# Kernel tuning notes

Hardware: AMD Instinct MI355X
Metric: run time of the kernel (lower is better)

The kernel has to match this reference:

```python
import jax, jax.numpy as jnp
import numpy as np

NH, NKV, HD = 32, 8, 64      # query heads, kv heads, head dim
H, INTER = 2048, 8192        # hidden, mlp intermediate
B, NBLK, BS = 32, 256, 16    # batch, blocks per seq, block size
NUM_BLOCKS = B * NBLK
EPS = 1e-5
THETA = 10000.0


def rms_norm(x, w):
    var = jnp.mean(x * x, axis=-1, keepdims=True)
    return x * jax.lax.rsqrt(var + EPS) * w


def rotate_half(x):
    x1, x2 = jnp.split(x, 2, axis=-1)
    return jnp.concatenate([-x2, x1], axis=-1)


def setup_inputs() -> dict:
    key = jax.random.key(0)
    ks = jax.random.split(key, 12)
    s = 0.02
    x = jax.random.normal(ks[0], (B, 1, H), jnp.float32)
    k_cache = jax.random.normal(ks[1], (NUM_BLOCKS, BS, NKV, HD), jnp.float32)
    v_cache = jax.random.normal(ks[2], (NUM_BLOCKS, BS, NKV, HD), jnp.float32)
    block_table = jnp.arange(B * NBLK, dtype=jnp.int32).reshape(B, NBLK)
    cache_seqlens = jax.random.randint(ks[3], (B,), 0, NBLK * BS - 1, jnp.int32)
    return {
        'x': x, 'k_cache': k_cache, 'v_cache': v_cache,
        'ln1_w': jnp.ones((H,), jnp.float32),
        'q_w': jax.random.normal(ks[4], (H, NH * HD), jnp.float32) * s,
        'k_w': jax.random.normal(ks[5], (H, NKV * HD), jnp.float32) * s,
        'v_w': jax.random.normal(ks[6], (H, NKV * HD), jnp.float32) * s,
        'o_w': jax.random.normal(ks[7], (NH * HD, H), jnp.float32) * s,
        'ln2_w': jnp.ones((H,), jnp.float32),
        'gate_w': jax.random.normal(ks[8], (H, INTER), jnp.float32) * s,
        'up_w': jax.random.normal(ks[9], (H, INTER), jnp.float32) * s,
        'down_w': jax.random.normal(ks[10], (INTER, H), jnp.float32) * s,
        'block_table': block_table,
        'cache_seqlens': cache_seqlens,
        'block_size': BS,
    }


def reference(x, k_cache, v_cache, ln1_w, q_w, k_w, v_w, o_w, ln2_w,
              gate_w, up_w, down_w, block_table, cache_seqlens, block_size):
    b = x.shape[0]
    normed = rms_norm(x, ln1_w)[:, 0, :]                     # [B,H]
    q = (normed @ q_w).reshape(b, NH, HD)                    # [B,NH,HD]
    k = (normed @ k_w).reshape(b, NKV, HD)                   # [B,NKV,HD]
    v = (normed @ v_w).reshape(b, NKV, HD)

    # RoPE at current position (HF rotate_half convention)
    pos = cache_seqlens.astype(jnp.float32)                  # [B]
    inv_freq = 1.0 / (THETA ** (jnp.arange(0, HD, 2, dtype=jnp.float32) / HD))
    ang = pos[:, None] * inv_freq[None, :]                   # [B,HD/2]
    cos = jnp.concatenate([jnp.cos(ang), jnp.cos(ang)], -1)[:, None, :]  # [B,1,HD]
    sin = jnp.concatenate([jnp.sin(ang), jnp.sin(ang)], -1)[:, None, :]
    q = q * cos + rotate_half(q) * sin
    k = k * cos + rotate_half(k) * sin

    # paged cache update: write new k/v at block_table[b, pos//bs], offset pos%bs
    blk = block_table[jnp.arange(b), cache_seqlens // block_size]
    flat_idx = blk.astype(jnp.int32) * block_size + cache_seqlens % block_size  # [B]
    kc = k_cache.reshape(-1, NKV, HD).at[flat_idx].set(k).reshape(k_cache.shape)
    vc = v_cache.reshape(-1, NKV, HD).at[flat_idx].set(v).reshape(v_cache.shape)

    # gather paged KV via block table -> [B, S, NKV, HD]
    K = kc[block_table].reshape(b, -1, NKV, HD)
    V = vc[block_table].reshape(b, -1, NKV, HD)
    S = K.shape[1]

    # decode attention with GQA: head h uses kv head h // (NH//NKV)
    G = NH // NKV
    qh = q.reshape(b, NKV, G, HD)
    scores = jnp.einsum('bkgd,bskd->bkgs', qh, K) / jnp.sqrt(jnp.float32(HD))
    valid = (jnp.arange(S)[None, :] <= cache_seqlens[:, None])  # seqlen+1 tokens
    scores = jnp.where(valid[:, None, None, :], scores, -jnp.inf)
    probs = jax.nn.softmax(scores, axis=-1)
    attn = jnp.einsum('bkgs,bskd->bkgd', probs, V).reshape(b, NH * HD)

    x = x + (attn @ o_w)[:, None, :]

    h = rms_norm(x, ln2_w)
    mlp = (jax.nn.silu(h @ gate_w) * (h @ up_w)) @ down_w
    return x + mlp
```

## Files before the change

kernel.cpp:

```cpp
#include <hip/hip_runtime.h>
#include <math.h>

#define B_      32
#define H_      2048
#define NH_     32
#define NKV_    8
#define HD_     64
#define G_      4
#define INTER_  8192
#define NBLK_   256
#define BS_     16
#define NCHUNK_ 8
#define CHUNK_  512

#define OFF_NORMED_T 0
#define OFF_QKV_P    65536
#define OFF_QROPE    1638400
#define OFF_HT       1703936
#define OFF_ATTN_T   1769472
#define OFF_GU_P     1835008
#define OFF_ACT_T    6029312
#define OFF_O_P      6291456
#define OFF_D_P      7340032
#define OFF_OPART    9437184
#define OFF_MPART    9961472
#define OFF_LPART    9969664

__global__ __launch_bounds__(256) void rmsnorm_kernel(const float* __restrict__ xin,
                                                      const float* __restrict__ w,
                                                      float* __restrict__ out_t) {
    int b = blockIdx.x, tid = threadIdx.x;
    const float* xr = xin + (size_t)b * H_;
    float xv[8];
    float ss = 0.f;
#pragma unroll
    for (int j = 0; j < 8; ++j) {
        xv[j] = xr[tid + j * 256];
        ss += xv[j] * xv[j];
    }
#pragma unroll
    for (int off = 32; off >= 1; off >>= 1) ss += __shfl_xor(ss, off, 64);
    __shared__ float red[4];
    __shared__ float rbc;
    if ((tid & 63) == 0) red[tid >> 6] = ss;
    __syncthreads();
    if (tid == 0) rbc = rsqrtf((red[0] + red[1] + red[2] + red[3]) / (float)H_ + 1e-5f);
    __syncthreads();
    float r = rbc;
#pragma unroll
    for (int j = 0; j < 8; ++j) {
        int i = tid + j * 256;
        out_t[(size_t)i * B_ + b] = xv[j] * r * w[i];
    }
}

__device__ __forceinline__ void gemv4_block(const float* __restrict__ xt,
                                            const float* __restrict__ W, int Nw,
                                            int wcol0, int rowsPerWave,
                                            float* __restrict__ part, int Nout,
                                            int outcol0) {
    int tid = threadIdx.x;
    int lane = tid & 63;
    int ks = tid >> 6;
    int k0 = (blockIdx.y * 4 + ks) * rowsPerWave;
    int wcol = wcol0 + lane * 4;

    float acc[4][B_];
#pragma unroll
    for (int c = 0; c < 4; ++c)
#pragma unroll
        for (int b = 0; b < B_; ++b) acc[c][b] = 0.f;

    const float* Wp = W + (size_t)k0 * Nw + wcol;
    const float* xp = xt + (size_t)k0 * B_;
#pragma unroll 2
    for (int k = 0; k < rowsPerWave; ++k) {
        float4 w4 = *(const float4*)(Wp + (size_t)k * Nw);
        const float* xr = xp + k * B_;
#pragma unroll
        for (int b = 0; b < B_; ++b) {
            float xv = xr[b];
            acc[0][b] = fmaf(w4.x, xv, acc[0][b]);
            acc[1][b] = fmaf(w4.y, xv, acc[1][b]);
            acc[2][b] = fmaf(w4.z, xv, acc[2][b]);
            acc[3][b] = fmaf(w4.w, xv, acc[3][b]);
        }
    }

    __shared__ float red[4][2][260];
    float* prow = part + (size_t)blockIdx.y * B_ * Nout;
    for (int b0 = 0; b0 < B_; b0 += 2) {
#pragma unroll
        for (int bi = 0; bi < 2; ++bi)
#pragma unroll
            for (int c = 0; c < 4; ++c)
                red[ks][bi][lane * 4 + c] = acc[c][b0 + bi];
        __syncthreads();
#pragma unroll
        for (int bi = 0; bi < 2; ++bi) {
            float s = red[0][bi][tid] + red[1][bi][tid] + red[2][bi][tid] + red[3][bi][tid];
            prow[(size_t)(b0 + bi) * Nout + outcol0 + tid] = s;
        }
        __syncthreads();
    }
}

__global__ __launch_bounds__(256, 2) void gemv_qkv_kernel(const float* __restrict__ xt,
                                                          const float* __restrict__ qw,
                                                          const float* __restrict__ kw,
                                                          const float* __restrict__ vw,
                                                          float* __restrict__ part) {
    int cb = blockIdx.x;
    if (cb < 8)       gemv4_block(xt, qw, 2048, cb * 256, 32, part, 3072, cb * 256);
    else if (cb < 10) gemv4_block(xt, kw, 512, (cb - 8) * 256, 32, part, 3072, cb * 256);
    else              gemv4_block(xt, vw, 512, (cb - 10) * 256, 32, part, 3072, cb * 256);
}

__global__ __launch_bounds__(256, 2) void gemv_o_kernel(const float* __restrict__ xt,
                                                        const float* __restrict__ W,
                                                        float* __restrict__ part) {
    gemv4_block(xt, W, 2048, blockIdx.x * 256, 32, part, 2048, blockIdx.x * 256);
}

__global__ __launch_bounds__(256, 2) void gemv_gateup_kernel(const float* __restrict__ xt,
                                                             const float* __restrict__ gw,
                                                             const float* __restrict__ uw,
                                                             float* __restrict__ part) {
    int cb = blockIdx.x;
    if (cb < 32) gemv4_block(xt, gw, 8192, cb * 256, 64, part, 16384, cb * 256);
    else         gemv4_block(xt, uw, 8192, (cb - 32) * 256, 64, part, 16384, 8192 + (cb - 32) * 256);
}

__global__ __launch_bounds__(256, 2) void gemv_down_kernel(const float* __restrict__ xt,
                                                           const float* __restrict__ W,
                                                           float* __restrict__ part) {
    gemv4_block(xt, W, 2048, blockIdx.x * 256, 64, part, 2048, blockIdx.x * 256);
}

__global__ __launch_bounds__(256) void qkv_reduce_rope_kernel(const float* __restrict__ part,
                                                              const int* __restrict__ btab,
                                                              const int* __restrict__ seql,
                                                              float* __restrict__ qrope,
                                                              float* __restrict__ kc,
                                                              float* __restrict__ vc) {
    int b = blockIdx.x, tid = threadIdx.x;
    __shared__ float s[3072];
#pragma unroll
    for (int j = 0; j < 12; ++j) {
        int col = tid + j * 256;
        float a = 0.f;
#pragma unroll
        for (int y = 0; y < 16; ++y) a += part[((size_t)y * B_ + b) * 3072 + col];
        s[col] = a;
    }
    __syncthreads();
    int pos = seql[b];
    float fpos = (float)pos;
    const float LOG2T = 13.287712379549449f;
#pragma unroll
    for (int j = 0; j < 8; ++j) {
        int i = tid + j * 256;
        int d = i & 63, ii = d & 31;
        float ang = fpos * exp2f(-(float)(2 * ii) * (LOG2T / 64.f));
        float c = cosf(ang), sn = sinf(ang);
        float v1 = s[i], v2 = s[(d < 32) ? i + 32 : i - 32];
        qrope[(size_t)b * 2048 + i] = (d < 32) ? (v1 * c - v2 * sn) : (v1 * c + v2 * sn);
    }
    int blk = btab[b * NBLK_ + (pos >> 4)];
    size_t cbase = (size_t)(blk * BS_ + (pos & 15)) * NKV_ * HD_;
    for (int i = tid; i < NKV_ * HD_; i += 256) {
        int d = i & 63, ii = d & 31;
        float ang = fpos * exp2f(-(float)(2 * ii) * (LOG2T / 64.f));
        float c = cosf(ang), sn = sinf(ang);
        float v1 = s[2048 + i], v2 = s[2048 + ((d < 32) ? i + 32 : i - 32)];
        kc[cbase + i] = (d < 32) ? (v1 * c - v2 * sn) : (v1 * c + v2 * sn);
        vc[cbase + i] = s[2560 + i];
    }
}

__global__ __launch_bounds__(256, 4) void attn_chunk_kernel(const float* __restrict__ qrope,
                                                            const float* __restrict__ kc,
                                                            const float* __restrict__ vc,
                                                            const int* __restrict__ btab,
                                                            const int* __restrict__ seqlens,
                                                            float* __restrict__ opart,
                                                            float* __restrict__ mpart,
                                                            float* __restrict__ lpart) {
    int cx = blockIdx.x, kv = blockIdx.y, b = blockIdx.z;
    int tid = threadIdx.x;
    int pos = seqlens[b];
    int c0 = cx * CHUNK_;
    int pidx = ((b * NKV_ + kv) * NCHUNK_ + cx) * G_;
    if (c0 > pos) {
        if (tid < G_) { mpart[pidx + tid] = -__builtin_inff(); lpart[pidx + tid] = 0.f; }
        return;
    }
    __shared__ float qlds[G_][HD_];
    __shared__ float slds[G_][CHUNK_];
    __shared__ float vt[32][HD_];
    __shared__ int btl[32];
    if (tid < 32) btl[tid] = btab[b * NBLK_ + (c0 >> 4) + tid];
    {
        int h = tid >> 6, d = tid & 63;
        qlds[h][d] = qrope[((size_t)b * NH_ + kv * G_ + h) * HD_ + d] * 0.125f;
    }
    __syncthreads();

    int grp = tid >> 4, ln = tid & 15;
    for (int tb = 0; tb < CHUNK_; tb += 16) {
        int tl = tb + grp;
        int t = c0 + tl;
        int blk = btl[tl >> 4];
        const float4 k4 = *(const float4*)(kc + ((size_t)(blk * BS_ + (t & 15)) * NKV_ + kv) * HD_ + ln * 4);
        bool valid = (t <= pos);
#pragma unroll
        for (int h = 0; h < G_; ++h) {
            const float4 q4 = *(const float4*)&qlds[h][ln * 4];
            float p = q4.x * k4.x + q4.y * k4.y + q4.z * k4.z + q4.w * k4.w;
#pragma unroll
            for (int off = 8; off >= 1; off >>= 1) p += __shfl_xor(p, off, 16);
            if (ln == 0) slds[h][tl] = valid ? p : -__builtin_inff();
        }
    }
    __syncthreads();

    int h = tid >> 6, lane = tid & 63;
    float m = -__builtin_inff();
    for (int i = lane; i < CHUNK_; i += 64) m = fmaxf(m, slds[h][i]);
#pragma unroll
    for (int off = 32; off >= 1; off >>= 1) m = fmaxf(m, __shfl_xor(m, off, 64));
    float l = 0.f;
    for (int i = lane; i < CHUNK_; i += 64) {
        float p = expf(slds[h][i] - m);
        slds[h][i] = p;
        l += p;
    }
#pragma unroll
    for (int off = 32; off >= 1; off >>= 1) l += __shfl_xor(l, off, 64);
    if (lane == 0) { mpart[pidx + h] = m; lpart[pidx + h] = l; }
    __syncthreads();

    int d = lane;
    float o = 0.f;
    int tmax = min(CHUNK_, pos + 1 - c0);
    for (int t0 = 0; t0 < tmax; t0 += 32) {
#pragma unroll
        for (int r = 0; r < 2; ++r) {
            int tl = t0 + r * 16 + (tid >> 4);
            int t = c0 + tl;
            int blk = btl[tl >> 4];
            *(float4*)&vt[r * 16 + (tid >> 4)][(tid & 15) * 4] =
                *(const float4*)(vc + ((size_t)(blk * BS_ + (t & 15)) * NKV_ + kv) * HD_ + (tid & 15) * 4);
        }
        __syncthreads();
#pragma unroll 8
        for (int tl2 = 0; tl2 < 32; ++tl2)
            o = fmaf(slds[h][t0 + tl2], vt[tl2][d], o);
        __syncthreads();
    }
    opart[(size_t)(pidx + h) * HD_ + d] = o;
}

__global__ __launch_bounds__(64) void attn_reduce_kernel(const float* __restrict__ opart,
                                                         const float* __restrict__ mpart,
                                                         const float* __restrict__ lpart,
                                                         float* __restrict__ attn_t) {
    int hq = blockIdx.x, b = blockIdx.y;
    int kv = hq >> 2, g = hq & 3;
    int lane = threadIdx.x;
    int base = ((b * NKV_ + kv) * NCHUNK_) * G_ + g;
    float mv[NCHUNK_], lv[NCHUNK_];
    float M = -__builtin_inff();
#pragma unroll
    for (int c = 0; c < NCHUNK_; ++c) {
        mv[c] = mpart[base + c * G_];
        lv[c] = lpart[base + c * G_];
        M = fmaxf(M, mv[c]);
    }
    float L = 0.f, o = 0.f;
#pragma unroll
    for (int c = 0; c < NCHUNK_; ++c) {
        if (lv[c] > 0.f) {
            float f = expf(mv[c] - M);
            L += lv[c] * f;
            o += f * opart[(size_t)(base + c * G_) * HD_ + lane];
        }
    }
    attn_t[(size_t)(hq * HD_ + lane) * B_ + b] = o / L;
}

__global__ __launch_bounds__(256) void o_reduce_rms2_kernel(const float* __restrict__ part,
                                                            const float* __restrict__ x,
                                                            const float* __restrict__ w2,
                                                            float* __restrict__ out,
                                                            float* __restrict__ ht) {
    int b = blockIdx.x, tid = threadIdx.x;
    float v[8];
    float ss = 0.f;
#pragma unroll
    for (int j = 0; j < 8; ++j) {
        int col = tid + j * 256;
        float a = x[(size_t)b * H_ + col];
#pragma unroll
        for (int y = 0; y < 16; ++y) a += part[((size_t)y * B_ + b) * 2048 + col];
        v[j] = a;
        ss += a * a;
    }
#pragma unroll
    for (int off = 32; off >= 1; off >>= 1) ss += __shfl_xor(ss, off, 64);
    __shared__ float red[4];
    __shared__ float rbc;
    if ((tid & 63) == 0) red[tid >> 6] = ss;
    __syncthreads();
    if (tid == 0) rbc = rsqrtf((red[0] + red[1] + red[2] + red[3]) / (float)H_ + 1e-5f);
    __syncthreads();
    float r = rbc;
#pragma unroll
    for (int j = 0; j < 8; ++j) {
        int col = tid + j * 256;
        out[(size_t)b * H_ + col] = v[j];
        ht[(size_t)col * B_ + b] = v[j] * r * w2[col];
    }
}

__global__ __launch_bounds__(256) void gu_reduce_silu_kernel(const float* __restrict__ part,
                                                             float* __restrict__ act_t) {
    int j0 = blockIdx.x * 64, tid = threadIdx.x;
    int jj = tid & 63, bq = tid >> 6;
    __shared__ float tile[64][33];
#pragma unroll
    for (int bb = 0; bb < 8; ++bb) {
        int b = bq * 8 + bb;
        float g = 0.f, u = 0.f;
#pragma unroll
        for (int y = 0; y < 8; ++y) {
            size_t base = ((size_t)y * B_ + b) * 16384 + j0 + jj;
            g += part[base];
            u += part[base + 8192];
        }
        tile[jj][b] = (g / (1.f + expf(-g))) * u;
    }
    __syncthreads();
#pragma unroll
    for (int r = 0; r < 8; ++r) {
        int j = r * 8 + (tid >> 5);
        int bc = tid & 31;
        act_t[(size_t)(j0 + j) * B_ + bc] = tile[j][bc];
    }
}

__global__ __launch_bounds__(256) void down_reduce_kernel(const float* __restrict__ part,
                                                          float* __restrict__ out) {
    int idx = blockIdx.x * 256 + threadIdx.x;
    float a = out[idx];
#pragma unroll
    for (int y = 0; y < 32; ++y) a += part[(size_t)y * 65536 + idx];
    out[idx] = a;
}

extern "C" void kernel_launch(void* const* d_in, const int* in_sizes, int n_in,
                              void* d_out, int out_size, void* d_ws, size_t ws_size,
                              hipStream_t stream) {
    const float* x       = (const float*)d_in[0];
    float*       k_cache = (float*)d_in[1];
    float*       v_cache = (float*)d_in[2];
    const float* ln1_w   = (const float*)d_in[3];
    const float* q_w     = (const float*)d_in[4];
    const float* k_w     = (const float*)d_in[5];
    const float* v_w     = (const float*)d_in[6];
    const float* o_w     = (const float*)d_in[7];
    const float* ln2_w   = (const float*)d_in[8];
    const float* gate_w  = (const float*)d_in[9];
    const float* up_w    = (const float*)d_in[10];
    const float* down_w  = (const float*)d_in[11];
    const int*   btab    = (const int*)d_in[12];
    const int*   seql    = (const int*)d_in[13];
    float* out = (float*)d_out;

    float* ws = (float*)d_ws;
    float* normed_t = ws + OFF_NORMED_T;
    float* qkv_p    = ws + OFF_QKV_P;
    float* qrope    = ws + OFF_QROPE;
    float* ht       = ws + OFF_HT;
    float* attn_t   = ws + OFF_ATTN_T;
    float* gu_p     = ws + OFF_GU_P;
    float* act_t    = ws + OFF_ACT_T;
    float* o_p      = ws + OFF_O_P;
    float* d_p      = ws + OFF_D_P;
    float* opart    = ws + OFF_OPART;
    float* mpart    = ws + OFF_MPART;
    float* lpart    = ws + OFF_LPART;

    rmsnorm_kernel<<<32, 256, 0, stream>>>(x, ln1_w, normed_t);
    gemv_qkv_kernel<<<dim3(12, 16), 256, 0, stream>>>(normed_t, q_w, k_w, v_w, qkv_p);
    qkv_reduce_rope_kernel<<<32, 256, 0, stream>>>(qkv_p, btab, seql, qrope, k_cache, v_cache);
    attn_chunk_kernel<<<dim3(NCHUNK_, NKV_, B_), 256, 0, stream>>>(qrope, k_cache, v_cache,
                                                                   btab, seql, opart, mpart, lpart);
    attn_reduce_kernel<<<dim3(NH_, B_), 64, 0, stream>>>(opart, mpart, lpart, attn_t);
    gemv_o_kernel<<<dim3(8, 16), 256, 0, stream>>>(attn_t, o_w, o_p);
    o_reduce_rms2_kernel<<<32, 256, 0, stream>>>(o_p, x, ln2_w, out, ht);
    gemv_gateup_kernel<<<dim3(64, 8), 256, 0, stream>>>(ht, gate_w, up_w, gu_p);
    gu_reduce_silu_kernel<<<128, 256, 0, stream>>>(gu_p, act_t);
    gemv_down_kernel<<<dim3(8, 32), 256, 0, stream>>>(act_t, down_w, d_p);
    down_reduce_kernel<<<256, 256, 0, stream>>>(d_p, out);
}
```

Before: 780.6 us.

## Vectorize loads across kernels, use packed FMA in GEMV, transpose V tile

Several kernels (rmsnorm, qkv reduce, o-reduce+rms2, down reduce) now use float4 loads and stores instead of scalar accesses, and down_reduce launches a quarter as many blocks. The shared GEMV core switches to 2-wide vector accumulators and packed FMA so the compiler can emit packed fp32 FMA instructions. The attention PV loop stores V transposed in padded LDS and reads probabilities and values as float4 into four independent accumulators. Together these aim to cut memory instruction count and ALU issue cost, with possible register pressure and LDS bank-conflict side effects.

```diff
diff --git a/kernel.cpp b/kernel.cpp
--- a/kernel.cpp
+++ b/kernel.cpp
@@ -12,6 +12,8 @@
 #define BS_     16
 #define NCHUNK_ 8
 #define CHUNK_  512
+
+typedef float v2f __attribute__((ext_vector_type(2)));
 
 #define OFF_NORMED_T 0
 #define OFF_QKV_P    65536
@@ -30,13 +32,14 @@
                                                       const float* __restrict__ w,
                                                       float* __restrict__ out_t) {
     int b = blockIdx.x, tid = threadIdx.x;
-    const float* xr = xin + (size_t)b * H_;
-    float xv[8];
+    const float4* xr4 = (const float4*)(xin + (size_t)b * H_);
+    float4 xv4[2];
     float ss = 0.f;
 #pragma unroll
-    for (int j = 0; j < 8; ++j) {
-        xv[j] = xr[tid + j * 256];
-        ss += xv[j] * xv[j];
+    for (int j = 0; j < 2; ++j) {
+        float4 t = xr4[tid + j * 256];
+        xv4[j] = t;
+        ss += t.x * t.x + t.y * t.y + t.z * t.z + t.w * t.w;
     }
 #pragma unroll
     for (int off = 32; off >= 1; off >>= 1) ss += __shfl_xor(ss, off, 64);
@@ -48,9 +51,13 @@
     __syncthreads();
     float r = rbc;
 #pragma unroll
-    for (int j = 0; j < 8; ++j) {
-        int i = tid + j * 256;
-        out_t[(size_t)i * B_ + b] = xv[j] * r * w[i];
+    for (int j = 0; j < 2; ++j) {
+        int col = (tid + j * 256) * 4;
+        const float4 w4 = *(const float4*)&w[col];
+        out_t[(size_t)(col + 0) * B_ + b] = xv4[j].x * r * w4.x;
+        out_t[(size_t)(col + 1) * B_ + b] = xv4[j].y * r * w4.y;
+        out_t[(size_t)(col + 2) * B_ + b] = xv4[j].z * r * w4.z;
+        out_t[(size_t)(col + 3) * B_ + b] = xv4[j].w * r * w4.w;
     }
 }
 
@@ -65,36 +72,42 @@
     int k0 = (blockIdx.y * 4 + ks) * rowsPerWave;
     int wcol = wcol0 + lane * 4;
 
-    float acc[4][B_];
+    v2f acc[4][16];
 #pragma unroll
     for (int c = 0; c < 4; ++c)
 #pragma unroll
-        for (int b = 0; b < B_; ++b) acc[c][b] = 0.f;
+        for (int b2 = 0; b2 < 16; ++b2) acc[c][b2] = (v2f)(0.f);
 
     const float* Wp = W + (size_t)k0 * Nw + wcol;
     const float* xp = xt + (size_t)k0 * B_;
 #pragma unroll 2
     for (int k = 0; k < rowsPerWave; ++k) {
         float4 w4 = *(const float4*)(Wp + (size_t)k * Nw);
+        v2f wa, wb, wc, wd;
+        wa.x = w4.x; wa.y = w4.x;
+        wb.x = w4.y; wb.y = w4.y;
+        wc.x = w4.z; wc.y = w4.z;
+        wd.x = w4.w; wd.y = w4.w;
         const float* xr = xp + k * B_;
 #pragma unroll
-        for (int b = 0; b < B_; ++b) {
-            float xv = xr[b];
-            acc[0][b] = fmaf(w4.x, xv, acc[0][b]);
-            acc[1][b] = fmaf(w4.y, xv, acc[1][b]);
-            acc[2][b] = fmaf(w4.z, xv, acc[2][b]);
-            acc[3][b] = fmaf(w4.w, xv, acc[3][b]);
+        for (int b2 = 0; b2 < 16; ++b2) {
+            v2f x2 = *(const v2f*)(xr + b2 * 2);
+            acc[0][b2] = __builtin_elementwise_fma(wa, x2, acc[0][b2]);
+            acc[1][b2] = __builtin_elementwise_fma(wb, x2, acc[1][b2]);
+            acc[2][b2] = __builtin_elementwise_fma(wc, x2, acc[2][b2]);
+            acc[3][b2] = __builtin_elementwise_fma(wd, x2, acc[3][b2]);
         }
     }
 
     __shared__ float red[4][2][260];
     float* prow = part + (size_t)blockIdx.y * B_ * Nout;
+#pragma unroll
     for (int b0 = 0; b0 < B_; b0 += 2) {
 #pragma unroll
         for (int bi = 0; bi < 2; ++bi)
 #pragma unroll
             for (int c = 0; c < 4; ++c)
-                red[ks][bi][lane * 4 + c] = acc[c][b0 + bi];
+                red[ks][bi][lane * 4 + c] = acc[c][b0 >> 1][bi];
         __syncthreads();
 #pragma unroll
         for (int bi = 0; bi < 2; ++bi) {
@@ -146,12 +159,15 @@
     int b = blockIdx.x, tid = threadIdx.x;
     __shared__ float s[3072];
 #pragma unroll
-    for (int j = 0; j < 12; ++j) {
-        int col = tid + j * 256;
-        float a = 0.f;
-#pragma unroll
-        for (int y = 0; y < 16; ++y) a += part[((size_t)y * B_ + b) * 3072 + col];
-        s[col] = a;
+    for (int j = 0; j < 3; ++j) {
+        int col = (tid + j * 256) * 4;
+        float4 a; a.x = 0.f; a.y = 0.f; a.z = 0.f; a.w = 0.f;
+#pragma unroll
+        for (int y = 0; y < 16; ++y) {
+            const float4 p = *(const float4*)&part[((size_t)y * B_ + b) * 3072 + col];
+            a.x += p.x; a.y += p.y; a.z += p.z; a.w += p.w;
+        }
+        *(float4*)&s[col] = a;
     }
     __syncthreads();
     int pos = seql[b];
@@ -197,7 +213,7 @@
     }
     __shared__ float qlds[G_][HD_];
     __shared__ float slds[G_][CHUNK_];
-    __shared__ float vt[32][HD_];
+    __shared__ float vtt[HD_][36];
     __shared__ int btl[32];
     if (tid < 32) btl[tid] = btab[b * NBLK_ + (c0 >> 4) + tid];
     {
@@ -241,7 +257,7 @@
     __syncthreads();
 
     int d = lane;
-    float o = 0.f;
+    float oa0 = 0.f, oa1 = 0.f, oa2 = 0.f, oa3 = 0.f;
     int tmax = min(CHUNK_, pos + 1 - c0);
     for (int t0 = 0; t0 < tmax; t0 += 32) {
 #pragma unroll
@@ -249,15 +265,28 @@
             int tl = t0 + r * 16 + (tid >> 4);
             int t = c0 + tl;
             int blk = btl[tl >> 4];
-            *(float4*)&vt[r * 16 + (tid >> 4)][(tid & 15) * 4] =
-                *(const float4*)(vc + ((size_t)(blk * BS_ + (t & 15)) * NKV_ + kv) * HD_ + (tid & 15) * 4);
+            const float4 vv = *(const float4*)(vc + ((size_t)(blk * BS_ + (t & 15)) * NKV_ + kv) * HD_ + (tid & 15) * 4);
+            int dd = (tid & 15) * 4, tc = r * 16 + (tid >> 4);
+            vtt[dd + 0][tc] = vv.x;
+            vtt[dd + 1][tc] = vv.y;
+            vtt[dd + 2][tc] = vv.z;
+            vtt[dd + 3][tc] = vv.w;
         }
         __syncthreads();
-#pragma unroll 8
-        for (int tl2 = 0; tl2 < 32; ++tl2)
-            o = fmaf(slds[h][t0 + tl2], vt[tl2][d], o);
+        {
+            float4 p4, v4;
+#define PV_STEP(tq, oacc) \
+            p4 = *(const float4*)&slds[h][t0 + (tq)]; \
+            v4 = *(const float4*)&vtt[d][(tq)]; \
+            oacc = fmaf(p4.x, v4.x, oacc); oacc = fmaf(p4.y, v4.y, oacc); \
+            oacc = fmaf(p4.z, v4.z, oacc); oacc = fmaf(p4.w, v4.w, oacc);
+            PV_STEP(0,  oa0) PV_STEP(4,  oa1) PV_STEP(8,  oa2) PV_STEP(12, oa3)
+            PV_STEP(16, oa0) PV_STEP(20, oa1) PV_STEP(24, oa2) PV_STEP(28, oa3)
+#undef PV_STEP
+        }
         __syncthreads();
     }
+    float o = (oa0 + oa1) + (oa2 + oa3);
     opart[(size_t)(pidx + h) * HD_ + d] = o;
 }
 
@@ -295,16 +324,19 @@
                                                             float* __restrict__ out,
                                                             float* __restrict__ ht) {
     int b = blockIdx.x, tid = threadIdx.x;
-    float v[8];
+    float4 v4[2];
     float ss = 0.f;
 #pragma unroll
-    for (int j = 0; j < 8; ++j) {
-        int col = tid + j * 256;
-        float a = x[(size_t)b * H_ + col];
-#pragma unroll
-        for (int y = 0; y < 16; ++y) a += part[((size_t)y * B_ + b) * 2048 + col];
-        v[j] = a;
-        ss += a * a;
+    for (int j = 0; j < 2; ++j) {
+        int col = (tid + j * 256) * 4;
+        float4 a = *(const float4*)&x[(size_t)b * H_ + col];
+#pragma unroll
+        for (int y = 0; y < 16; ++y) {
+            const float4 p = *(const float4*)&part[((size_t)y * B_ + b) * 2048 + col];
+            a.x += p.x; a.y += p.y; a.z += p.z; a.w += p.w;
+        }
+        v4[j] = a;
+        ss += a.x * a.x + a.y * a.y + a.z * a.z + a.w * a.w;
     }
 #pragma unroll
     for (int off = 32; off >= 1; off >>= 1) ss += __shfl_xor(ss, off, 64);
@@ -316,10 +348,14 @@
     __syncthreads();
     float r = rbc;
 #pragma unroll
-    for (int j = 0; j < 8; ++j) {
-        int col = tid + j * 256;
-        out[(size_t)b * H_ + col] = v[j];
-        ht[(size_t)col * B_ + b] = v[j] * r * w2[col];
+    for (int j = 0; j < 2; ++j) {
+        int col = (tid + j * 256) * 4;
+        *(float4*)&out[(size_t)b * H_ + col] = v4[j];
+        const float4 w4 = *(const float4*)&w2[col];
+        ht[(size_t)(col + 0) * B_ + b] = v4[j].x * r * w4.x;
+        ht[(size_t)(col + 1) * B_ + b] = v4[j].y * r * w4.y;
+        ht[(size_t)(col + 2) * B_ + b] = v4[j].z * r * w4.z;
+        ht[(size_t)(col + 3) * B_ + b] = v4[j].w * r * w4.w;
     }
 }
 
@@ -351,11 +387,14 @@
 
 __global__ __launch_bounds__(256) void down_reduce_kernel(const float* __restrict__ part,
                                                           float* __restrict__ out) {
-    int idx = blockIdx.x * 256 + threadIdx.x;
-    float a = out[idx];
-#pragma unroll
-    for (int y = 0; y < 32; ++y) a += part[(size_t)y * 65536 + idx];
-    out[idx] = a;
+    int idx = (blockIdx.x * 256 + threadIdx.x) * 4;
+    float4 a = *(const float4*)&out[idx];
+#pragma unroll
+    for (int y = 0; y < 32; ++y) {
+        const float4 p = *(const float4*)&part[(size_t)y * 65536 + idx];
+        a.x += p.x; a.y += p.y; a.z += p.z; a.w += p.w;
+    }
+    *(float4*)&out[idx] = a;
 }
 
 extern "C" void kernel_launch(void* const* d_in, const int* in_sizes, int n_in,
@@ -402,5 +441,5 @@
     gemv_gateup_kernel<<<dim3(64, 8), 256, 0, stream>>>(ht, gate_w, up_w, gu_p);
     gu_reduce_silu_kernel<<<128, 256, 0, stream>>>(gu_p, act_t);
     gemv_down_kernel<<<dim3(8, 32), 256, 0, stream>>>(act_t, down_w, d_p);
-    down_reduce_kernel<<<256, 256, 0, stream>>>(d_p, out);
-}
+    down_reduce_kernel<<<64, 256, 0, stream>>>(d_p, out);
+}
```

Measured after the change: 785.2 us. No clear change (+0.6%).
